# Optimization experiments

Hardware: AMD Instinct MI355X
Metric: run time of the kernel (lower is better)

The kernel has to match this reference:

```python
import jax, jax.numpy as jnp
import numpy as np

N = 200000   # num nodes
E = 2500000  # num edges
H = 32       # hidden_dim
EPS = 1e-5   # BatchNorm eps


def _gcn_conv(x, W, b, src, dst, norm):
    # GCNConv: D^{-1/2}(A+I)D^{-1/2} X W + b  (self-loops folded in via norm^2 term)
    h = x @ W                                   # [N, H_out]
    coef = norm[src] * norm[dst]                # [E]
    msg = h[src] * coef[:, None]                # [E, H_out] -- dominant HBM traffic
    agg = jax.ops.segment_sum(msg, dst, num_segments=N)
    agg = agg + h * (norm * norm)[:, None]      # self-loop contribution
    return agg + b


def _bn(x, gamma, beta):
    # BatchNorm1d in training mode: batch statistics over the node dimension
    m = jnp.mean(x, axis=0)
    v = jnp.var(x, axis=0)
    return gamma * (x - m) * jax.lax.rsqrt(v + EPS) + beta


def setup_inputs() -> dict:
    key = jax.random.key(0)
    ks = jax.random.split(key, 12)
    x = jax.random.uniform(ks[0], (N, 1), dtype=jnp.float32) * 50.0  # degree-like feature
    edge_index = jax.random.randint(ks[1], (2, E), 0, N, dtype=jnp.int64)
    edge_attr = jax.random.normal(ks[2], (E,), dtype=jnp.float32)
    s = 0.1
    return {
        'x': x, 'edge_index': edge_index, 'edge_attr': edge_attr,
        'W1': jax.random.normal(ks[3], (1, H), dtype=jnp.float32) * s,
        'b1': jnp.zeros((H,), jnp.float32),
        'g1': jnp.ones((H,), jnp.float32), 'be1': jnp.zeros((H,), jnp.float32),
        'W2': jax.random.normal(ks[4], (H, H), dtype=jnp.float32) * s,
        'b2': jnp.zeros((H,), jnp.float32),
        'g2': jnp.ones((H,), jnp.float32), 'be2': jnp.zeros((H,), jnp.float32),
        'W3': jax.random.normal(ks[5], (H, H), dtype=jnp.float32) * s,
        'b3': jnp.zeros((H,), jnp.float32),
        'g3': jnp.ones((H,), jnp.float32), 'be3': jnp.zeros((H,), jnp.float32),
        'fcW': jax.random.normal(ks[6], (H, 1), dtype=jnp.float32) * s,
        'fcb': jnp.zeros((1,), jnp.float32),
    }


def reference(x, edge_index, edge_attr, W1, b1, g1, be1, W2, b2, g2, be2,
              W3, b3, g3, be3, fcW, fcb):
    src, dst = edge_index[0], edge_index[1]
    # symmetric normalization from degrees of A + I
    deg = jax.ops.segment_sum(jnp.ones((E,), x.dtype), dst, num_segments=N) + 1.0
    norm = jax.lax.rsqrt(deg)                   # deg^{-1/2}, [N]

    h = jax.nn.relu(_bn(_gcn_conv(x, W1, b1, src, dst, norm), g1, be1))
    h = jax.nn.relu(_bn(_gcn_conv(h, W2, b2, src, dst, norm), g2, be2))
    h = jax.nn.relu(_bn(_gcn_conv(h, W3, b3, src, dst, norm), g3, be3))
    # dropout is identity in eval / deterministic reference
    return h @ fcW + fcb                        # [N, 1]
```

## Files before the change

### kernel.cpp

```cpp
#include <hip/hip_runtime.h>
#include <hip/hip_bf16.h>
#include <hip/hip_fp16.h>

#define N_NODES 200000
#define N_EDGES 2500000
#define HID 32
#define BN_EPS 1e-5f

#define BKT_SHIFT 10
#define B_BKT ((N_NODES + 1023) / 1024)
#define PAD 16
#define CAPB 14336
#define EDGES_PER_BLK 8192
#define NB_SCAT ((N_EDGES + EDGES_PER_BLK - 1) / EDGES_PER_BLK)

#define SBANK 4096
#define SSTR 16
#define S1SUM 0
#define S1SQ  16
#define L2SUM 32
#define L2SQ  544
#define L3SUM 1056
#define L3SQ  1568

#define NB1  3125
#define NBL2 3125
#define ITL2 2
#define NBH  3125

__device__ __forceinline__ void atomAddF(float* p, float v) {
    unsafeAtomicAdd(p, v);
}

__global__ void k_init(int* __restrict__ bcur16, float* __restrict__ stats) {
    int i = blockIdx.x * blockDim.x + threadIdx.x;
    if (i < B_BKT * PAD) bcur16[i] = 0;
    if (i < 4 * SBANK) stats[i] = 0.0f;
}

__global__ void __launch_bounds__(1024)
k_scatter(const int* __restrict__ ei, int* __restrict__ bcur16,
          unsigned int* __restrict__ ebuf) {
    __shared__ int lh[B_BKT], lbase[B_BKT], lc[B_BKT];
    int t = threadIdx.x;
    if (t < B_BKT) { lh[t] = 0; lc[t] = 0; }
    __syncthreads();
    int base = blockIdx.x * EDGES_PER_BLK;
    int sv[8], dv[8];
#pragma unroll
    for (int k = 0; k < 8; k++) {
        int e = base + k * 1024 + t;
        if (e < N_EDGES) {
            sv[k] = ei[e];
            dv[k] = ei[N_EDGES + e];
            atomicAdd(&lh[dv[k] >> BKT_SHIFT], 1);
        } else dv[k] = -1;
    }
    __syncthreads();
    if (t < B_BKT) lbase[t] = lh[t] ? atomicAdd(&bcur16[t * PAD], lh[t]) : 0;
    __syncthreads();
#pragma unroll
    for (int k = 0; k < 8; k++) {
        if (dv[k] >= 0) {
            int b = dv[k] >> BKT_SHIFT;
            int loc = atomicAdd(&lc[b], 1);
            ebuf[(size_t)b * CAPB + lbase[b] + loc] =
                ((unsigned)(dv[k] & 1023) << 18) | (unsigned)sv[k];
        }
    }
}

__global__ void __launch_bounds__(1024)
k_bucket(const unsigned int* __restrict__ ebuf, const int* __restrict__ bcur16,
         const float* __restrict__ x, int* __restrict__ rowbeg,
         int* __restrict__ cntg, float* __restrict__ norm,
         float* __restrict__ xp, int* __restrict__ csrc) {
    __shared__ int hist[1024], rbase[1024];
    __shared__ int wsum[16];
    int b = blockIdx.x;
    int t = threadIdx.x;
    int lane = t & 63, wv = t >> 6;
    int count = bcur16[b * PAD];
    size_t ebase = (size_t)b * CAPB;
    int nbase = b << BKT_SHIFT;
    hist[t] = 0;
    __syncthreads();
    for (int i = t; i < count; i += 1024)
        atomicAdd(&hist[ebuf[ebase + i] >> 18], 1);
    __syncthreads();
    int v = hist[t];
    int val = v;
#pragma unroll
    for (int off = 1; off < 64; off <<= 1) {
        int nn = __shfl_up(val, off);
        if (lane >= off) val += nn;
    }
    if (lane == 63) wsum[wv] = val;
    __syncthreads();
    if (t < 16) {
        int wval = wsum[t];
        int wincl = wval;
#pragma unroll
        for (int off = 1; off < 16; off <<= 1) {
            int nn = __shfl_up(wincl, off, 16);
            if (t >= off) wincl += nn;
        }
        wsum[t] = wincl - wval;
    }
    __syncthreads();
    int excl = (val - v) + wsum[wv];
    int rb = b * CAPB + excl;
    rbase[t] = rb;
    int n = nbase + t;
    if (n < N_NODES) {
        rowbeg[n] = rb;
        cntg[n] = v;
        float nm = rsqrtf((float)v + 1.0f);
        norm[n] = nm;
        xp[n] = x[n] * nm;
    }
    __syncthreads();
    hist[t] = 0;
    __syncthreads();
    for (int i = t; i < count; i += 1024) {
        unsigned int w = ebuf[ebase + i];
        int ld = w >> 18;
        int loc = atomicAdd(&hist[ld], 1);
        csrc[rbase[ld] + loc] = (int)(w & 0x3FFFFu);
    }
}

__global__ void __launch_bounds__(256)
k_gather1(const int* __restrict__ rowbeg, const int* __restrict__ cntg,
          const int* __restrict__ csrc, const float* __restrict__ xp,
          const float* __restrict__ norm, float2* __restrict__ sn2,
          float* __restrict__ stats) {
    __shared__ float ls[256], lq[256];
    int tid = threadIdx.x;
    int nl = tid >> 2, q = tid & 3;
    int n = blockIdx.x * 64 + nl;
    int beg = rowbeg[n], dg = cntg[n];
    float A0 = 0.f, A1 = 0.f;
    int i = q;
    for (; i + 4 < dg; i += 8) {
        A0 += xp[csrc[beg + i]];
        A1 += xp[csrc[beg + i + 4]];
    }
    if (i < dg) A0 += xp[csrc[beg + i]];
    float acc = A0 + A1;
    acc += __shfl_xor(acc, 1);
    acc += __shfl_xor(acc, 2);
    float val = 0.f;
    if (q == 0) {
        acc += xp[n];
        float nm = norm[n];
        val = nm * acc;
        sn2[n] = make_float2(val, nm);
    }
    ls[tid] = val; lq[tid] = val * val;
    __syncthreads();
    for (int off = 128; off; off >>= 1) {
        if (tid < (unsigned)off) { ls[tid] += ls[tid + off]; lq[tid] += lq[tid + off]; }
        __syncthreads();
    }
    if (tid == 0) {
        int bo = (blockIdx.x & 3) * SBANK;
        atomAddF(&stats[bo + S1SUM], ls[0]);
        atomAddF(&stats[bo + S1SQ],  lq[0]);
    }
}

#define PHI(aa, bb, pp) ((pp).y * fmaxf(fmaf((aa), (pp).x, (bb)), 0.f))

__global__ void __launch_bounds__(256)
k_layer2(const int* __restrict__ rowbeg, const int* __restrict__ cntg,
         const int* __restrict__ csrc, const float2* __restrict__ sn2,
         const float* __restrict__ stats, const float* __restrict__ W1,
         const float* __restrict__ g1, const float* __restrict__ be1,
         const float* __restrict__ W2, float* __restrict__ B,
         float* __restrict__ sumO, float* __restrict__ sqO) {
    __shared__ float w2s[1024];
    __shared__ float ajs[32], bjs[32];
    __shared__ float yx[32][36];
    __shared__ float red[4][8][8];
    int tid = threadIdx.x;
    for (int i = tid; i < 1024; i += 256) w2s[i] = W2[i];
    if (tid < 32) {
        float sm = stats[S1SUM] + stats[SBANK + S1SUM] +
                   stats[2*SBANK + S1SUM] + stats[3*SBANK + S1SUM];
        float sq = stats[S1SQ] + stats[SBANK + S1SQ] +
                   stats[2*SBANK + S1SQ] + stats[3*SBANK + S1SQ];
        float m   = sm * (1.0f / N_NODES);
        float var = sq * (1.0f / N_NODES) - m * m;
        float w = W1[tid];
        float a = g1[tid] * w * rsqrtf(var * w * w + BN_EPS);
        ajs[tid] = a;
        bjs[tid] = be1[tid] - m * a;
    }
    __syncthreads();
    int nl = tid >> 3, cg = (tid & 7) * 4;
    float a0 = ajs[cg], a1 = ajs[cg+1], a2 = ajs[cg+2], a3 = ajs[cg+3];
    float b0 = bjs[cg], b1 = bjs[cg+1], b2 = bjs[cg+2], b3 = bjs[cg+3];
    float s0=0,s1=0,s2=0,s3=0,q0=0,q1=0,q2=0,q3=0;
#pragma unroll
    for (int it = 0; it < ITL2; it++) {
        int n = (it * NBL2 + blockIdx.x) * 32 + nl;
        int beg = rowbeg[n], dg = cntg[n];
        float2 self = sn2[n];
        float nm = self.y;
        float h0 = PHI(a0,b0,self), h1 = PHI(a1,b1,self),
              h2 = PHI(a2,b2,self), h3 = PHI(a3,b3,self);
        int i = 0;
        for (; i + 3 < dg; i += 4) {
            int e0 = csrc[beg+i],   e1 = csrc[beg+i+1],
                e2 = csrc[beg+i+2], e3 = csrc[beg+i+3];
            float2 p0 = sn2[e0], p1 = sn2[e1], p2 = sn2[e2], p3 = sn2[e3];
            h0 += PHI(a0,b0,p0) + PHI(a0,b0,p1) + PHI(a0,b0,p2) + PHI(a0,b0,p3);
            h1 += PHI(a1,b1,p0) + PHI(a1,b1,p1) + PHI(a1,b1,p2) + PHI(a1,b1,p3);
            h2 += PHI(a2,b2,p0) + PHI(a2,b2,p1) + PHI(a2,b2,p2) + PHI(a2,b2,p3);
            h3 += PHI(a3,b3,p0) + PHI(a3,b3,p1) + PHI(a3,b3,p2) + PHI(a3,b3,p3);
        }
        for (; i < dg; i++) {
            float2 p = sn2[csrc[beg + i]];
            h0 += PHI(a0,b0,p); h1 += PHI(a1,b1,p);
            h2 += PHI(a2,b2,p); h3 += PHI(a3,b3,p);
        }
        __syncthreads();
        *(float4*)&yx[nl][cg] = make_float4(h0,h1,h2,h3);
        __syncthreads();
        float o0=0,o1=0,o2=0,o3=0;
#pragma unroll
        for (int k = 0; k < 32; k += 4) {
            float4 hh  = *(const float4*)&yx[nl][k];
            float4 wr0 = *(const float4*)&w2s[(k+0)*32 + cg];
            float4 wr1 = *(const float4*)&w2s[(k+1)*32 + cg];
            float4 wr2 = *(const float4*)&w2s[(k+2)*32 + cg];
            float4 wr3 = *(const float4*)&w2s[(k+3)*32 + cg];
            o0 = fmaf(hh.x,wr0.x, fmaf(hh.y,wr1.x, fmaf(hh.z,wr2.x, fmaf(hh.w,wr3.x, o0))));
            o1 = fmaf(hh.x,wr0.y, fmaf(hh.y,wr1.y, fmaf(hh.z,wr2.y, fmaf(hh.w,wr3.y, o1))));
            o2 = fmaf(hh.x,wr0.z, fmaf(hh.y,wr1.z, fmaf(hh.z,wr2.z, fmaf(hh.w,wr3.z, o2))));
            o3 = fmaf(hh.x,wr0.w, fmaf(hh.y,wr1.w, fmaf(hh.z,wr2.w, fmaf(hh.w,wr3.w, o3))));
        }
        o0 *= nm; o1 *= nm; o2 *= nm; o3 *= nm;
        *(float4*)(B + (size_t)n * 32 + cg) = make_float4(o0,o1,o2,o3);
        s0 += o0; s1 += o1; s2 += o2; s3 += o3;
        q0 += o0*o0; q1 += o1*o1; q2 += o2*o2; q3 += o3*o3;
    }
#pragma unroll
    for (int mask = 32; mask >= 8; mask >>= 1) {
        s0 += __shfl_xor(s0, mask); s1 += __shfl_xor(s1, mask);
        s2 += __shfl_xor(s2, mask); s3 += __shfl_xor(s3, mask);
        q0 += __shfl_xor(q0, mask); q1 += __shfl_xor(q1, mask);
        q2 += __shfl_xor(q2, mask); q3 += __shfl_xor(q3, mask);
    }
    int wv = tid >> 6, ln = tid & 63;
    if (ln < 8) {
        float* r = red[wv][ln];
        r[0]=s0; r[1]=s1; r[2]=s2; r[3]=s3;
        r[4]=q0; r[5]=q1; r[6]=q2; r[7]=q3;
    }
    __syncthreads();
    if (tid < 8) {
        float tacc[8] = {0,0,0,0,0,0,0,0};
#pragma unroll
        for (int w = 0; w < 4; w++)
#pragma unroll
            for (int k = 0; k < 8; k++) tacc[k] += red[w][tid][k];
        int cb = tid * 4;
        int bo = (blockIdx.x & 3) * SBANK;
#pragma unroll
        for (int k = 0; k < 4; k++) {
            atomAddF(&sumO[bo + (cb + k) * SSTR], tacc[k]);
            atomAddF(&sqO [bo + (cb + k) * SSTR], tacc[4 + k]);
        }
    }
}

__global__ void __launch_bounds__(256)
k_fusedB(const float* __restrict__ norm, const float* __restrict__ sum,
         const float* __restrict__ sumsq, const float* __restrict__ g,
         const float* __restrict__ be, const float* __restrict__ W,
         const float* __restrict__ aggIn, __half* __restrict__ hOut) {
    __shared__ float wl[1024];
    __shared__ float scs[32], shs[32];
    __shared__ float yx[32][36];
    int tid = threadIdx.x;
    for (int i = tid; i < 1024; i += 256) wl[i] = W[i];
    if (tid < 32) {
        int o = tid * SSTR;
        float sm = sum[o] + sum[o+SBANK] + sum[o+2*SBANK] + sum[o+3*SBANK];
        float sq = sumsq[o] + sumsq[o+SBANK] + sumsq[o+2*SBANK] + sumsq[o+3*SBANK];
        float m   = sm * (1.0f / N_NODES);
        float var = sq * (1.0f / N_NODES) - m * m;
        float scj = g[tid] * rsqrtf(var + BN_EPS);
        scs[tid] = scj;
        shs[tid] = be[tid] - m * scj;
    }
    __syncthreads();
    int nl = tid >> 3, cg = (tid & 7) * 4;
    int n = blockIdx.x * 32 + nl;
    float4 bi = *(const float4*)(aggIn + (size_t)n * 32 + cg);
    float y0 = fmaxf(scs[cg  ]*bi.x + shs[cg  ], 0.f);
    float y1 = fmaxf(scs[cg+1]*bi.y + shs[cg+1], 0.f);
    float y2 = fmaxf(scs[cg+2]*bi.z + shs[cg+2], 0.f);
    float y3 = fmaxf(scs[cg+3]*bi.w + shs[cg+3], 0.f);
    *(float4*)&yx[nl][cg] = make_float4(y0,y1,y2,y3);
    __syncthreads();
    float o0=0,o1=0,o2=0,o3=0;
#pragma unroll
    for (int k = 0; k < 32; k += 4) {
        float4 hh  = *(const float4*)&yx[nl][k];
        float4 wr0 = *(const float4*)&wl[(k+0)*32 + cg];
        float4 wr1 = *(const float4*)&wl[(k+1)*32 + cg];
        float4 wr2 = *(const float4*)&wl[(k+2)*32 + cg];
        float4 wr3 = *(const float4*)&wl[(k+3)*32 + cg];
        o0 = fmaf(hh.x,wr0.x, fmaf(hh.y,wr1.x, fmaf(hh.z,wr2.x, fmaf(hh.w,wr3.x, o0))));
        o1 = fmaf(hh.x,wr0.y, fmaf(hh.y,wr1.y, fmaf(hh.z,wr2.y, fmaf(hh.w,wr3.y, o1))));
        o2 = fmaf(hh.x,wr0.z, fmaf(hh.y,wr1.z, fmaf(hh.z,wr2.z, fmaf(hh.w,wr3.z, o2))));
        o3 = fmaf(hh.x,wr0.w, fmaf(hh.y,wr1.w, fmaf(hh.z,wr2.w, fmaf(hh.w,wr3.w, o3))));
    }
    float nm = norm[n];
    __half2 ha = __floats2half2_rn(o0 * nm, o1 * nm);
    __half2 hb = __floats2half2_rn(o2 * nm, o3 * nm);
    float2 pk;
    ((__half2*)&pk)[0] = ha;
    ((__half2*)&pk)[1] = hb;
    *(float2*)(hOut + (size_t)n * 32 + cg) = pk;
}

__device__ __forceinline__ void load8h(const __half* p, float2& f0, float2& f1,
                                       float2& f2, float2& f3) {
    float4 raw = *(const float4*)p;
    const __half2* h = (const __half2*)&raw;
    f0 = __half22float2(h[0]);
    f1 = __half22float2(h[1]);
    f2 = __half22float2(h[2]);
    f3 = __half22float2(h[3]);
}

__global__ void __launch_bounds__(256)
k_gatherH(const int* __restrict__ rowbeg, const int* __restrict__ cntg,
          const int* __restrict__ csrc, const __half* __restrict__ A,
          const float* __restrict__ norm, float* __restrict__ B,
          float* __restrict__ sum, float* __restrict__ sumsq) {
    int tid = threadIdx.x;
    int nl = tid >> 2;
    int c8 = (tid & 3) * 8;
    int n = blockIdx.x * 64 + nl;
    int beg = rowbeg[n], dg = cntg[n];
    float2 a0, a1, a2, a3;
    load8h(A + (size_t)n * 32 + c8, a0, a1, a2, a3);
    int i = 0;
    for (; i + 1 < dg; i += 2) {
        int e0 = csrc[beg + i], e1 = csrc[beg + i + 1];
        float2 b0, b1, b2, b3, c0, c1, c2, c3;
        load8h(A + (size_t)e0 * 32 + c8, b0, b1, b2, b3);
        load8h(A + (size_t)e1 * 32 + c8, c0, c1, c2, c3);
        a0.x += b0.x + c0.x; a0.y += b0.y + c0.y;
        a1.x += b1.x + c1.x; a1.y += b1.y + c1.y;
        a2.x += b2.x + c2.x; a2.y += b2.y + c2.y;
        a3.x += b3.x + c3.x; a3.y += b3.y + c3.y;
    }
    if (i < dg) {
        float2 b0, b1, b2, b3;
        load8h(A + (size_t)csrc[beg + i] * 32 + c8, b0, b1, b2, b3);
        a0.x += b0.x; a0.y += b0.y; a1.x += b1.x; a1.y += b1.y;
        a2.x += b2.x; a2.y += b2.y; a3.x += b3.x; a3.y += b3.y;
    }
    float nm = norm[n];
    float o[8] = {a0.x * nm, a0.y * nm, a1.x * nm, a1.y * nm,
                  a2.x * nm, a2.y * nm, a3.x * nm, a3.y * nm};
    *(float4*)(B + (size_t)n * 32 + c8)     = make_float4(o[0], o[1], o[2], o[3]);
    *(float4*)(B + (size_t)n * 32 + c8 + 4) = make_float4(o[4], o[5], o[6], o[7]);
    float st[16];
#pragma unroll
    for (int k = 0; k < 8; k++) { st[k] = o[k]; st[8 + k] = o[k] * o[k]; }
#pragma unroll
    for (int mask = 32; mask >= 4; mask >>= 1)
#pragma unroll
        for (int k = 0; k < 16; k++) st[k] += __shfl_xor(st[k], mask);
    __shared__ float red[4][4][16];
    int wv = tid >> 6, ln = tid & 63;
    if (ln < 4) {
#pragma unroll
        for (int k = 0; k < 16; k++) red[wv][ln][k] = st[k];
    }
    __syncthreads();
    if (tid < 4) {
        float tacc[16];
#pragma unroll
        for (int k = 0; k < 16; k++) tacc[k] = 0.f;
#pragma unroll
        for (int w = 0; w < 4; w++)
#pragma unroll
            for (int k = 0; k < 16; k++) tacc[k] += red[w][tid][k];
        int cb = tid * 8;
        int bo = (blockIdx.x & 3) * SBANK;
#pragma unroll
        for (int k = 0; k < 8; k++) {
            atomAddF(&sum[bo + (cb + k) * SSTR], tacc[k]);
            atomAddF(&sumsq[bo + (cb + k) * SSTR], tacc[8 + k]);
        }
    }
}

__global__ void __launch_bounds__(256)
k_final(const float* __restrict__ aggIn, const float* __restrict__ sum,
        const float* __restrict__ sumsq, const float* __restrict__ g,
        const float* __restrict__ be, const float* __restrict__ fcW,
        const float* __restrict__ fcb, float* __restrict__ out) {
    __shared__ float scs[32], shs[32], fws[32];
    int tid = threadIdx.x;
    if (tid < 32) {
        int o = tid * SSTR;
        float sm = sum[o] + sum[o+SBANK] + sum[o+2*SBANK] + sum[o+3*SBANK];
        float sq = sumsq[o] + sumsq[o+SBANK] + sumsq[o+2*SBANK] + sumsq[o+3*SBANK];
        float m   = sm * (1.0f / N_NODES);
        float var = sq * (1.0f / N_NODES) - m * m;
        float scj = g[tid] * rsqrtf(var + BN_EPS);
        scs[tid] = scj;
        shs[tid] = be[tid] - m * scj;
        fws[tid] = fcW[tid];
    }
    __syncthreads();
    int nl = tid >> 3, cg = (tid & 7) * 4;
    int n = blockIdx.x * 32 + nl;
    float4 bi = *(const float4*)(aggIn + (size_t)n * 32 + cg);
    float v = fmaxf(scs[cg  ]*bi.x + shs[cg  ], 0.f) * fws[cg  ]
            + fmaxf(scs[cg+1]*bi.y + shs[cg+1], 0.f) * fws[cg+1]
            + fmaxf(scs[cg+2]*bi.z + shs[cg+2], 0.f) * fws[cg+2]
            + fmaxf(scs[cg+3]*bi.w + shs[cg+3], 0.f) * fws[cg+3];
    v += __shfl_xor(v, 1);
    v += __shfl_xor(v, 2);
    v += __shfl_xor(v, 4);
    if ((tid & 7) == 0) out[n] = v + fcb[0];
}

extern "C" void kernel_launch(void* const* d_in, const int* in_sizes, int n_in,
                              void* d_out, int out_size, void* d_ws, size_t ws_size,
                              hipStream_t stream) {
    const float* x   = (const float*)d_in[0];
    const int*   ei  = (const int*)d_in[1];
    const float* W1  = (const float*)d_in[3];
    const float* g1  = (const float*)d_in[5];
    const float* be1 = (const float*)d_in[6];
    const float* W2  = (const float*)d_in[7];
    const float* g2  = (const float*)d_in[9];
    const float* be2 = (const float*)d_in[10];
    const float* W3  = (const float*)d_in[11];
    const float* g3  = (const float*)d_in[13];
    const float* be3 = (const float*)d_in[14];
    const float* fcW = (const float*)d_in[15];
    const float* fcb = (const float*)d_in[16];
    float* out = (float*)d_out;

    char* base = (char*)d_ws;
    __half*       A16  = (__half*)base;
    unsigned int* ebuf = (unsigned int*)base;
    float*  B      = (float*)(base + (size_t)N_NODES * 32 * 4);
    int*    csrc   = (int*)(base + (size_t)N_NODES * 32 * 8);
    int*    rowbeg = csrc + (size_t)B_BKT * CAPB;
    int*    cntg   = rowbeg + N_NODES;
    float*  norm   = (float*)(cntg + N_NODES);
    float*  xp     = norm + N_NODES;
    float2* sn2    = (float2*)(xp + N_NODES);
    float*  stats  = (float*)(sn2 + N_NODES);
    int*    bcur16 = (int*)(stats + 4 * SBANK);

    k_init   <<<64, 256, 0, stream>>>(bcur16, stats);
    k_scatter<<<NB_SCAT, 1024, 0, stream>>>(ei, bcur16, ebuf);
    k_bucket <<<B_BKT, 1024, 0, stream>>>(ebuf, bcur16, x, rowbeg, cntg, norm, xp, csrc);
    k_gather1<<<NB1, 256, 0, stream>>>(rowbeg, cntg, csrc, xp, norm, sn2, stats);
    k_layer2 <<<NBL2, 256, 0, stream>>>(rowbeg, cntg, csrc, sn2, stats,
                                        W1, g1, be1, W2, B,
                                        stats + L2SUM, stats + L2SQ);
    k_fusedB <<<6250, 256, 0, stream>>>(norm, stats + L2SUM, stats + L2SQ,
                                        g2, be2, W3, B, A16);
    k_gatherH<<<NBH, 256, 0, stream>>>(rowbeg, cntg, csrc, A16, norm, B,
                                       stats + L3SUM, stats + L3SQ);
    k_final  <<<6250, 256, 0, stream>>>(B, stats + L3SUM, stats + L3SQ,
                                        g3, be3, fcW, fcb, out);
}
```

Before: 312.9 us.

## Sort CSR neighbor lists and use nontemporal loads/stores in gather kernels

Adds a per-row insertion sort of source indices after CSR construction so that neighbour gathers touch memory in ascending order. It also switches the CSR index reads to nontemporal loads and the float output stores to nontemporal stores, so streamed data does not evict reusable gather data from cache. The half-precision gather loop is unrolled from 2 to 4 edges to put more loads in flight. The insertion sort runs serially, one thread per row, and degrees are uneven, so it adds work to the CSR build kernel.

```diff
diff --git a/kernel.cpp b/kernel.cpp
--- a/kernel.cpp
+++ b/kernel.cpp
@@ -28,8 +28,15 @@
 #define ITL2 2
 #define NBH  3125
 
+typedef float nfloat4 __attribute__((ext_vector_type(4)));
+
 __device__ __forceinline__ void atomAddF(float* p, float v) {
     unsafeAtomicAdd(p, v);
+}
+
+__device__ __forceinline__ void ntStore4(float* p, float a, float b, float c, float d) {
+    nfloat4 v = {a, b, c, d};
+    __builtin_nontemporal_store(v, (nfloat4*)p);
 }
 
 __global__ void k_init(int* __restrict__ bcur16, float* __restrict__ stats) {
@@ -128,6 +135,16 @@
         int loc = atomicAdd(&hist[ld], 1);
         csrc[rbase[ld] + loc] = (int)(w & 0x3FFFFu);
     }
+    __syncthreads();
+    for (int a = 1; a < v; a++) {
+        int key = csrc[rb + a];
+        int p = a - 1;
+        while (p >= 0 && csrc[rb + p] > key) {
+            csrc[rb + p + 1] = csrc[rb + p];
+            p--;
+        }
+        csrc[rb + p + 1] = key;
+    }
 }
 
 __global__ void __launch_bounds__(256)
@@ -143,10 +160,10 @@
     float A0 = 0.f, A1 = 0.f;
     int i = q;
     for (; i + 4 < dg; i += 8) {
-        A0 += xp[csrc[beg + i]];
-        A1 += xp[csrc[beg + i + 4]];
-    }
-    if (i < dg) A0 += xp[csrc[beg + i]];
+        A0 += xp[__builtin_nontemporal_load(csrc + beg + i)];
+        A1 += xp[__builtin_nontemporal_load(csrc + beg + i + 4)];
+    }
+    if (i < dg) A0 += xp[__builtin_nontemporal_load(csrc + beg + i)];
     float acc = A0 + A1;
     acc += __shfl_xor(acc, 1);
     acc += __shfl_xor(acc, 2);
@@ -212,8 +229,10 @@
               h2 = PHI(a2,b2,self), h3 = PHI(a3,b3,self);
         int i = 0;
         for (; i + 3 < dg; i += 4) {
-            int e0 = csrc[beg+i],   e1 = csrc[beg+i+1],
-                e2 = csrc[beg+i+2], e3 = csrc[beg+i+3];
+            int e0 = __builtin_nontemporal_load(csrc + beg + i);
+            int e1 = __builtin_nontemporal_load(csrc + beg + i + 1);
+            int e2 = __builtin_nontemporal_load(csrc + beg + i + 2);
+            int e3 = __builtin_nontemporal_load(csrc + beg + i + 3);
             float2 p0 = sn2[e0], p1 = sn2[e1], p2 = sn2[e2], p3 = sn2[e3];
             h0 += PHI(a0,b0,p0) + PHI(a0,b0,p1) + PHI(a0,b0,p2) + PHI(a0,b0,p3);
             h1 += PHI(a1,b1,p0) + PHI(a1,b1,p1) + PHI(a1,b1,p2) + PHI(a1,b1,p3);
@@ -221,7 +240,7 @@
             h3 += PHI(a3,b3,p0) + PHI(a3,b3,p1) + PHI(a3,b3,p2) + PHI(a3,b3,p3);
         }
         for (; i < dg; i++) {
-            float2 p = sn2[csrc[beg + i]];
+            float2 p = sn2[__builtin_nontemporal_load(csrc + beg + i)];
             h0 += PHI(a0,b0,p); h1 += PHI(a1,b1,p);
             h2 += PHI(a2,b2,p); h3 += PHI(a3,b3,p);
         }
@@ -242,7 +261,7 @@
             o3 = fmaf(hh.x,wr0.w, fmaf(hh.y,wr1.w, fmaf(hh.z,wr2.w, fmaf(hh.w,wr3.w, o3))));
         }
         o0 *= nm; o1 *= nm; o2 *= nm; o3 *= nm;
-        *(float4*)(B + (size_t)n * 32 + cg) = make_float4(o0,o1,o2,o3);
+        ntStore4(B + (size_t)n * 32 + cg, o0, o1, o2, o3);
         s0 += o0; s1 += o1; s2 += o2; s3 += o3;
         q0 += o0*o0; q1 += o1*o1; q2 += o2*o2; q3 += o3*o3;
     }
@@ -328,14 +347,14 @@
     *(float2*)(hOut + (size_t)n * 32 + cg) = pk;
 }
 
-__device__ __forceinline__ void load8h(const __half* p, float2& f0, float2& f1,
-                                       float2& f2, float2& f3) {
-    float4 raw = *(const float4*)p;
+__device__ __forceinline__ void acc8(float* a, float4 raw) {
     const __half2* h = (const __half2*)&raw;
-    f0 = __half22float2(h[0]);
-    f1 = __half22float2(h[1]);
-    f2 = __half22float2(h[2]);
-    f3 = __half22float2(h[3]);
+    float2 f0 = __half22float2(h[0]);
+    float2 f1 = __half22float2(h[1]);
+    float2 f2 = __half22float2(h[2]);
+    float2 f3 = __half22float2(h[3]);
+    a[0] += f0.x; a[1] += f0.y; a[2] += f1.x; a[3] += f1.y;
+    a[4] += f2.x; a[5] += f2.y; a[6] += f3.x; a[7] += f3.y;
 }
 
 __global__ void __launch_bounds__(256)
@@ -348,30 +367,39 @@
     int c8 = (tid & 3) * 8;
     int n = blockIdx.x * 64 + nl;
     int beg = rowbeg[n], dg = cntg[n];
-    float2 a0, a1, a2, a3;
-    load8h(A + (size_t)n * 32 + c8, a0, a1, a2, a3);
+    const __half* Ac = A + c8;
+    float acc[8] = {0,0,0,0,0,0,0,0};
+    acc8(acc, *(const float4*)(Ac + (size_t)n * 32));
     int i = 0;
-    for (; i + 1 < dg; i += 2) {
-        int e0 = csrc[beg + i], e1 = csrc[beg + i + 1];
-        float2 b0, b1, b2, b3, c0, c1, c2, c3;
-        load8h(A + (size_t)e0 * 32 + c8, b0, b1, b2, b3);
-        load8h(A + (size_t)e1 * 32 + c8, c0, c1, c2, c3);
-        a0.x += b0.x + c0.x; a0.y += b0.y + c0.y;
-        a1.x += b1.x + c1.x; a1.y += b1.y + c1.y;
-        a2.x += b2.x + c2.x; a2.y += b2.y + c2.y;
-        a3.x += b3.x + c3.x; a3.y += b3.y + c3.y;
+    for (; i + 3 < dg; i += 4) {
+        int e0 = __builtin_nontemporal_load(csrc + beg + i);
+        int e1 = __builtin_nontemporal_load(csrc + beg + i + 1);
+        int e2 = __builtin_nontemporal_load(csrc + beg + i + 2);
+        int e3 = __builtin_nontemporal_load(csrc + beg + i + 3);
+        float4 r0 = *(const float4*)(Ac + (size_t)e0 * 32);
+        float4 r1 = *(const float4*)(Ac + (size_t)e1 * 32);
+        float4 r2 = *(const float4*)(Ac + (size_t)e2 * 32);
+        float4 r3 = *(const float4*)(Ac + (size_t)e3 * 32);
+        acc8(acc, r0); acc8(acc, r1); acc8(acc, r2); acc8(acc, r3);
+    }
+    if (i + 1 < dg) {
+        int e0 = __builtin_nontemporal_load(csrc + beg + i);
+        int e1 = __builtin_nontemporal_load(csrc + beg + i + 1);
+        float4 r0 = *(const float4*)(Ac + (size_t)e0 * 32);
+        float4 r1 = *(const float4*)(Ac + (size_t)e1 * 32);
+        acc8(acc, r0); acc8(acc, r1);
+        i += 2;
     }
     if (i < dg) {
-        float2 b0, b1, b2, b3;
-        load8h(A + (size_t)csrc[beg + i] * 32 + c8, b0, b1, b2, b3);
-        a0.x += b0.x; a0.y += b0.y; a1.x += b1.x; a1.y += b1.y;
-        a2.x += b2.x; a2.y += b2.y; a3.x += b3.x; a3.y += b3.y;
+        int e0 = __builtin_nontemporal_load(csrc + beg + i);
+        acc8(acc, *(const float4*)(Ac + (size_t)e0 * 32));
     }
     float nm = norm[n];
-    float o[8] = {a0.x * nm, a0.y * nm, a1.x * nm, a1.y * nm,
-                  a2.x * nm, a2.y * nm, a3.x * nm, a3.y * nm};
-    *(float4*)(B + (size_t)n * 32 + c8)     = make_float4(o[0], o[1], o[2], o[3]);
-    *(float4*)(B + (size_t)n * 32 + c8 + 4) = make_float4(o[4], o[5], o[6], o[7]);
+    float o[8];
+#pragma unroll
+    for (int k = 0; k < 8; k++) o[k] = acc[k] * nm;
+    ntStore4(B + (size_t)n * 32 + c8,     o[0], o[1], o[2], o[3]);
+    ntStore4(B + (size_t)n * 32 + c8 + 4, o[4], o[5], o[6], o[7]);
     float st[16];
 #pragma unroll
     for (int k = 0; k < 8; k++) { st[k] = o[k]; st[8 + k] = o[k] * o[k]; }
```

After: 413.3 us. 1.32x slower.
